# Performance work log

Hardware: AMD Instinct MI355X
Metric: run time of the kernel (lower is better)

## Reference

```python
import jax, jax.numpy as jnp
import numpy as np

B, OBS, H, N = 16384, 512, 1024, 9

def setup_inputs() -> dict:
    key = jax.random.key(0)
    ks = jax.random.split(key, 12)
    s = 0.02
    return {
        "obs": jax.random.normal(ks[0], (B, OBS), jnp.float32),
        "agent_positions": jax.random.normal(ks[1], (B, N, 3), jnp.float32),
        "W1": jax.random.normal(ks[2], (OBS, H), jnp.float32) * s,
        "b1": jnp.zeros((H,), jnp.float32),
        "W2": jax.random.normal(ks[3], (H, H), jnp.float32) * s,
        "b2": jnp.zeros((H,), jnp.float32),
        "Wc1": jax.random.normal(ks[4], (H, H // 2), jnp.float32) * s,
        "bc1": jnp.zeros((H // 2,), jnp.float32),
        "Wc2": jax.random.normal(ks[5], (H // 2, 1), jnp.float32) * s,
        "bc2": jnp.zeros((1,), jnp.float32),
        "Wt1": jax.random.normal(ks[6], (H, H // 2), jnp.float32) * s,
        "bt1": jnp.zeros((H // 2,), jnp.float32),
        "Wt2": jax.random.normal(ks[7], (H // 2, 1), jnp.float32) * s,
        "bt2": jnp.zeros((1,), jnp.float32),
        "Wk1": jax.random.normal(ks[8], (2 * H, H), jnp.float32) * s,
        "bk1": jnp.zeros((H,), jnp.float32),
        "Wk2": jax.random.normal(ks[9], (H, 1), jnp.float32) * s,
        "bk2": jnp.zeros((1,), jnp.float32),
    }


def reference(obs, agent_positions, W1, b1, W2, b2, Wc1, bc1, Wc2, bc2,
              Wt1, bt1, Wt2, bt2, Wk1, bk1, Wk2, bk2):
    # global features: Linear->ReLU->Linear->ReLU
    g = jax.nn.relu(obs @ W1 + b1)
    g = jax.nn.relu(g @ W2 + b2)  # [B, H]

    # Each per-agent head is applied to the SAME g in the original loop,
    # so one pass + broadcast is mathematically identical.
    cov = jax.nn.sigmoid(jax.nn.relu(g @ Wc1 + bc1) @ Wc2 + bc2)  # [B,1]
    trk = jax.nn.sigmoid(jax.nn.relu(g @ Wt1 + bt1) @ Wt2 + bt2)  # [B,1]
    coop_in = jnp.concatenate([g, g], axis=-1)                    # [B,2H]
    coop = jax.nn.sigmoid(jax.nn.relu(coop_in @ Wk1 + bk1) @ Wk2 + bk2)  # [B,1]
    # mean over 8 identical cooperation scores == the score itself

    coverage = jnp.broadcast_to(cov, (cov.shape[0], N))      # [B, N]
    tracking = jnp.broadcast_to(trk, (trk.shape[0], N))      # [B, N]
    cooperation = jnp.broadcast_to(coop, (coop.shape[0], N)) # [B, N]
    return (coverage, tracking, cooperation)
```

## Files before the change

### kernel.cpp

```cpp
#include <hip/hip_runtime.h>
#include <hip/hip_bf16.h>

#define B_ROWS 16384
#define OBS_D  512
#define H_D    1024
#define N_AG   9

typedef __attribute__((ext_vector_type(8))) short short8;
typedef __attribute__((ext_vector_type(4))) float floatx4;

__device__ __forceinline__ unsigned short f_to_bf_raw(float f) {
  union { float f; unsigned u; } c; c.f = f;
  unsigned u = c.u;
  u = u + 0x7FFF + ((u >> 16) & 1);
  return (unsigned short)(u >> 16);
}

__device__ __forceinline__ size_t frag_off(int n, int k, int KT32) {
  const int ft = (n >> 4) * KT32 + (k >> 5);
  const int ln = (n & 15) | (((k >> 3) & 3) << 4);
  return ((size_t)ft * 64 + ln) * 8 + (k & 7);
}

__global__ __launch_bounds__(256) void prep_all(
    const float* __restrict__ obs,
    const float* __restrict__ W1, const float* __restrict__ W2,
    const float* __restrict__ Wc1, const float* __restrict__ Wt1,
    const float* __restrict__ Wk1,
    const float* __restrict__ bc1, const float* __restrict__ bt1,
    const float* __restrict__ bk1,
    const float* __restrict__ Wc2, const float* __restrict__ Wt2,
    const float* __restrict__ Wk2,
    unsigned short* __restrict__ obs_bf,
    unsigned short* __restrict__ W1f, unsigned short* __restrict__ W2f,
    unsigned short* __restrict__ WHf,
    float* __restrict__ bias2048, float* __restrict__ w2cat) {
  __shared__ float t[32][33];
  const int bx  = blockIdx.x;
  const int tid = threadIdx.x;

  if (bx < 4096) {
    int i = (bx * 256 + tid) * 8;
    float4 a = *(const float4*)(obs + i);
    float4 b = *(const float4*)(obs + i + 4);
    short8 o;
    o[0] = (short)f_to_bf_raw(a.x); o[1] = (short)f_to_bf_raw(a.y);
    o[2] = (short)f_to_bf_raw(a.z); o[3] = (short)f_to_bf_raw(a.w);
    o[4] = (short)f_to_bf_raw(b.x); o[5] = (short)f_to_bf_raw(b.y);
    o[6] = (short)f_to_bf_raw(b.z); o[7] = (short)f_to_bf_raw(b.w);
    *(short8*)(obs_bf + i) = o;
    return;
  }

  const int tx = tid & 31;
  const int ty = tid >> 5;

  if (bx < 4608) {
    const int tt = bx - 4096;
    const int k0 = (tt & 15) * 32;
    const int n0 = (tt >> 4) * 32;
#pragma unroll
    for (int i = ty; i < 32; i += 8)
      t[i][tx] = W1[(size_t)(k0 + i) * 1024 + n0 + tx];
    __syncthreads();
#pragma unroll
    for (int i = ty; i < 32; i += 8)
      W1f[frag_off(n0 + i, k0 + tx, 16)] = f_to_bf_raw(t[tx][i]);
    return;
  }

  if (bx < 5632) {
    const int tt = bx - 4608;
    const int k0 = (tt & 31) * 32;
    const int n0 = (tt >> 5) * 32;
#pragma unroll
    for (int i = ty; i < 32; i += 8)
      t[i][tx] = W2[(size_t)(k0 + i) * 1024 + n0 + tx];
    __syncthreads();
#pragma unroll
    for (int i = ty; i < 32; i += 8)
      W2f[frag_off(n0 + i, k0 + tx, 32)] = f_to_bf_raw(t[tx][i]);
    return;
  }

  if (bx < 7680) {
    const int tt = bx - 5632;
    const int k0 = (tt & 31) * 32;
    const int n0 = (tt >> 5) * 32;
#pragma unroll
    for (int i = ty; i < 32; i += 8) {
      const int n = n0 + tx;
      float v;
      if (n0 < 512)
        v = Wc1[(size_t)(k0 + i) * 512 + n];
      else if (n0 < 1024)
        v = Wt1[(size_t)(k0 + i) * 512 + (n - 512)];
      else
        v = Wk1[(size_t)(k0 + i) * 1024 + (n - 1024)]
          + Wk1[(size_t)(k0 + i + 1024) * 1024 + (n - 1024)];
      t[i][tx] = v;
    }
    __syncthreads();
#pragma unroll
    for (int i = ty; i < 32; i += 8)
      WHf[frag_off(n0 + i, k0 + tx, 32)] = f_to_bf_raw(t[tx][i]);
    return;
  }

  {
    int n = (bx - 7680) * 256 + tid;
    float b, w;
    if (n < 512)       { b = bc1[n];        w = Wc2[n]; }
    else if (n < 1024) { b = bt1[n - 512];  w = Wt2[n - 512]; }
    else               { b = bk1[n - 1024]; w = Wk2[n - 1024]; }
    bias2048[n] = b;
    w2cat[n] = w;
  }
}

#define GLD_LDS(gp, lp)                                                        \
  __builtin_amdgcn_global_load_lds(                                            \
      (const __attribute__((address_space(1))) void*)(gp),                     \
      (__attribute__((address_space(3))) void*)(lp), 16, 0, 0)

#define SCB __builtin_amdgcn_sched_barrier(0)

#define MFMA_BF16(a, b, c) __builtin_amdgcn_mfma_f32_16x16x32_bf16(a, b, c, 0, 0, 0)

#define GEMM_CORE_V9(ACC_DECL)                                                 \
  __shared__ __align__(16) unsigned short As[3][128 * 64];          \
  const int tid  = threadIdx.x;                                                \
  const int lane = tid & 63;                                                   \
  const int wave = tid >> 6;                                                   \
  const int m0 = blockIdx.x * 128;                                             \
  const int n0 = blockIdx.y * 128;                                             \
  const int wm = (wave & 1) * 64;                                              \
  const int wn = (wave >> 1) * 64;                                             \
  const int fr = lane & 15;                                                    \
  const int fq = lane >> 4;                                                    \
  ACC_DECL;                                                                    \
  constexpr int KT   = K >> 6;                      \
  constexpr int KT32 = K >> 5;                      \
  const size_t rowb = (size_t)K * 2;                                           \
  const int srow8  = lane >> 3;                   \
  const int schunk = (lane & 7) ^ srow8;          \
  const char* gA = (const char*)A + (size_t)(m0 + wave * 32 + srow8) * rowb    \
                   + schunk * 16;                                              \
  char* lA = (char*)&As[0][0] + wave * 4096 + lane * 16;                       \
  const unsigned short* gB =                                                   \
      Bf + ((size_t)(((n0 + wn) >> 4) * KT32) * 64 + lane) * 8;                \
  const int fsA = (wm + fr) * 128;                                             \
  const int sl0 = ((fq)     ^ (fr & 7)) * 16;                                  \
  const int sl1 = ((4 + fq) ^ (fr & 7)) * 16;                                  \
  short8 FbP[2][2][4];                                                         \
  _Pragma("unroll")                                                            \
  for (int j = 0; j < 4; ++j)                                                  \
    GLD_LDS(gA + (size_t)j * 8 * rowb, lA + j * 1024);                         \
  _Pragma("unroll")                                                            \
  for (int j = 0; j < 4; ++j)                                                  \
    GLD_LDS(gA + 128 + (size_t)j * 8 * rowb,                                   \
            (char*)&As[1][0] + wave * 4096 + lane * 16 + j * 1024);            \
  _Pragma("unroll")                                                            \
  for (int s = 0; s < 2; ++s)                                                  \
    _Pragma("unroll")                                                          \
    for (int ni = 0; ni < 4; ++ni)                                             \
      FbP[0][s][ni] = *(const short8*)(gB + ((size_t)ni * KT32 + s) * 512);    \
  _Pragma("unroll")                                                            \
  for (int k = 0; k < KT; ++k) {           \
    __syncthreads();            \
    if (k + 2 < KT) {                                                          \
      char* d = (char*)&As[(k + 2) % 3][0] + wave * 4096 + lane * 16;          \
      const char* g = gA + (size_t)(k + 2) * 128;                              \
      _Pragma("unroll")                                                        \
      for (int j = 0; j < 4; ++j)                                              \
        GLD_LDS(g + (size_t)j * 8 * rowb, d + j * 1024);                       \
    }                                                                          \
    if (k + 1 < KT) {                                                          \
      _Pragma("unroll")                                                        \
      for (int s = 0; s < 2; ++s)                                              \
        _Pragma("unroll")                                                      \
        for (int ni = 0; ni < 4; ++ni)                                         \
          FbP[(k + 1) & 1][s][ni] = *(const short8*)                           \
              (gB + ((size_t)ni * KT32 + 2 * (k + 1) + s) * 512);              \
    }                                                                          \
    const char* bA = (const char*)&As[k % 3][0];                               \
    short8 Fa0[4], Fa1[4];                                                     \
    _Pragma("unroll")                                                          \
    for (int mi = 0; mi < 4; ++mi)                                             \
      Fa0[mi] = *(const short8*)(bA + fsA + mi * 2048 + sl0);                  \
    _Pragma("unroll")                                                          \
    for (int mi = 0; mi < 4; ++mi)                                             \
      Fa1[mi] = *(const short8*)(bA + fsA + mi * 2048 + sl1);                  \
    _Pragma("unroll")                                                          \
    for (int mi = 0; mi < 4; ++mi)                                             \
      _Pragma("unroll")                                                        \
      for (int ni = 0; ni < 4; ++ni)                                           \
        acc[mi][ni] = __builtin_amdgcn_mfma_f32_16x16x32_bf16(                 \
            Fa0[mi], FbP[k & 1][0][ni], acc[mi][ni], 0, 0, 0);                 \
    _Pragma("unroll")                                                          \
    for (int mi = 0; mi < 4; ++mi)                                             \
      _Pragma("unroll")                                                        \
      for (int ni = 0; ni < 4; ++ni)                                           \
        acc[mi][ni] = __builtin_amdgcn_mfma_f32_16x16x32_bf16(                 \
            Fa1[mi], FbP[k & 1][1][ni], acc[mi][ni], 0, 0, 0);                 \
  }

#define ACC_INIT4                                                              \
  floatx4 acc[4][4];                                                           \
  _Pragma("unroll")                                                            \
  for (int i = 0; i < 4; ++i)                                                  \
    _Pragma("unroll")                                                          \
    for (int j = 0; j < 4; ++j) acc[i][j] = (floatx4){0.f, 0.f, 0.f, 0.f}

#define ST_A16(T, kh)                                                          \
  GLD_LDS(gA0 + (size_t)(T) * 128 + (kh) * 64,                                 \
          Lds + ((T) & 1) * 65536 + (kh) * 16384 + lA0);                       \
  GLD_LDS(gA1 + (size_t)(T) * 128 + (kh) * 64,                                 \
          Lds + ((T) & 1) * 65536 + (kh) * 16384 + lA0 + 8192)

#define ST_B16(T, kh)                                                          \
  GLD_LDS(gB0 + (size_t)(2 * (T) + (kh)) * 1024,                               \
          Lds + ((T) & 1) * 65536 + (kh) * 16384 + lB0);                       \
  GLD_LDS(gB1 + (size_t)(2 * (T) + (kh)) * 1024,                               \
          Lds + ((T) & 1) * 65536 + (kh) * 16384 + lB0 + 8192)

#define ROW16(mi, FA)                                                          \
  acc[mi][0] = MFMA_BF16(FA, Fb0v, acc[mi][0]);                                \
  acc[mi][1] = MFMA_BF16(FA, Fb1v, acc[mi][1]);                                \
  acc[mi][2] = MFMA_BF16(FA, Fb2v, acc[mi][2]);                                \
  acc[mi][3] = MFMA_BF16(FA, Fb3v, acc[mi][3])

#define PHASE16(TT, ks, STAGE_STMT, PRE_BAR2)                                  \
  {                                                                            \
    const char* pb = Lds + ((TT) & 1) * 65536 + (ks) * 16384;                  \
    short8 Fa0 = *(const short8*)(pb + faB + 0 * 1024);                        \
    short8 Fa1 = *(const short8*)(pb + faB + 1 * 1024);                        \
    short8 Fa2 = *(const short8*)(pb + faB + 2 * 1024);                        \
    short8 Fa3 = *(const short8*)(pb + faB + 3 * 1024);                        \
    short8 Fa4 = *(const short8*)(pb + faB + 4 * 1024);                        \
    short8 Fa5 = *(const short8*)(pb + faB + 5 * 1024);                        \
    short8 Fa6 = *(const short8*)(pb + faB + 6 * 1024);                        \
    short8 Fa7 = *(const short8*)(pb + faB + 7 * 1024);                        \
    short8 Fb0v = *(const short8*)(pb + fbB);                                  \
    short8 Fb1v = *(const short8*)(pb + fbB + 1024);                           \
    short8 Fb2v = *(const short8*)(pb + fbB + 2048);                           \
    short8 Fb3v = *(const short8*)(pb + fbB + 3072);                           \
    STAGE_STMT;                                                                \
    SCB; __builtin_amdgcn_s_barrier(); SCB;                                    \
    __builtin_amdgcn_s_setprio(1);                                             \
    ROW16(0, Fa0); ROW16(1, Fa1); ROW16(2, Fa2); ROW16(3, Fa3);                \
    ROW16(4, Fa4); ROW16(5, Fa5); ROW16(6, Fa6); ROW16(7, Fa7);                \
    __builtin_amdgcn_s_setprio(0);                                             \
    PRE_BAR2;                                                                  \
    SCB; __builtin_amdgcn_s_barrier(); SCB;                                    \
  }

#define GEMM_CORE_V16(ACC_DECL)                                                \
  __shared__ __align__(16) char Lds[131072];                                   \
  const int tid  = threadIdx.x;                                                \
  const int lane = tid & 63;                                                   \
  const int wave = tid >> 6;                                         \
  const int m0 = blockIdx.x * 256;                                             \
  const int n0 = blockIdx.y * 256;                                             \
  const int wm = (wave & 1) * 128;                  \
  const int wn = (wave >> 1) * 64;                                             \
  const int fr = lane & 15;                                                    \
  const int fq = lane >> 4;                                                    \
  ACC_DECL;                                                                    \
  constexpr int KT   = K >> 6;                                                 \
  constexpr int KT32 = K >> 5;                                                 \
  const size_t rowb = (size_t)K * 2;                                           \
  const char* gA0 = (const char*)A                                             \
      + (size_t)(m0 + wave * 16 + (lane >> 2)) * rowb                          \
      + (((lane & 3) ^ ((lane >> 3) & 3)) * 16);                               \
  const char* gA1 = gA0 + (size_t)128 * rowb;                                  \
  const char* gB0 = (const char*)Bf                                            \
      + ((size_t)((n0 >> 4) + wave) * KT32) * 1024 + lane * 16;                \
  const char* gB1 = gB0 + (size_t)8 * KT32 * 1024;                             \
  const int lA0 = wave * 1024 + lane * 16;                                     \
  const int lB0 = 32768 + wave * 1024 + lane * 16;                             \
  const int faB = (wm + fr) * 64 + ((fq ^ ((fr >> 1) & 3)) * 16);              \
  const int fbB = 32768 + ((wave >> 1) * 4) * 1024 + lane * 16;                \
               \
  ST_A16(0, 0); ST_B16(0, 0); ST_A16(0, 1); ST_B16(0, 1);                      \
  SCB;                                                                         \
  ST_A16(1, 0); ST_B16(1, 0);                                                  \
  SCB;                                                                         \
  asm volatile("s_waitcnt vmcnt(4)" ::: "memory");       \
  __builtin_amdgcn_s_barrier();                  \
  SCB;                                                                         \
  _Pragma("unroll")                                                            \
  for (int T = 0; T < KT; ++T) {           \
    PHASE16(T, 0,                                                              \
            { if (T + 1 < KT) { ST_A16(T + 1, 1); ST_B16(T + 1, 1); } },       \
            (void)0);                                                          \
    PHASE16(T, 1,                                                              \
            { if (T + 2 < KT) { ST_A16(T + 2, 0); ST_B16(T + 2, 0); } },       \
            if (T + 1 < KT) {                                                  \
              SCB;                                                             \
              if (T + 2 < KT) {                                                \
                asm volatile("s_waitcnt vmcnt(4)" ::: "memory");               \
              } else {                                                         \
                asm volatile("s_waitcnt vmcnt(0)" ::: "memory");               \
              }                                                                \
              SCB;                                                             \
            });                                                                \
  }

#define ACC_INIT8                                                              \
  floatx4 acc[8][4];                                                           \
  _Pragma("unroll")                                                            \
  for (int i = 0; i < 8; ++i)                                                  \
    _Pragma("unroll")                                                          \
    for (int j = 0; j < 4; ++j) acc[i][j] = (floatx4){0.f, 0.f, 0.f, 0.f}

template <int K>
__global__ __launch_bounds__(256, 2) void gemm_bias_relu(
    const unsigned short* __restrict__ A,
    const unsigned short* __restrict__ Bf,
    const float* __restrict__ bias,
    unsigned short* __restrict__ C,
    int M, int N) {
  GEMM_CORE_V9(ACC_INIT4)

#pragma unroll
  for (int ni = 0; ni < 4; ++ni) {
    const int gn = n0 + wn + ni * 16 + fr;
    const float bv = bias[gn];
#pragma unroll
    for (int mi = 0; mi < 4; ++mi) {
#pragma unroll
      for (int r = 0; r < 4; ++r) {
        const int gm = m0 + wm + mi * 16 + fq * 4 + r;
        float v = acc[mi][ni][r] + bv;
        v = v > 0.f ? v : 0.f;
        C[(size_t)gm * N + gn] = f_to_bf_raw(v);
      }
    }
  }
}

template <int K>
__global__ __launch_bounds__(512, 2) void gemm_heads_fused(
    const unsigned short* __restrict__ A,
    const unsigned short* __restrict__ Bf,
    const float* __restrict__ bias,
    const float* __restrict__ w2,
    float* __restrict__ part,
    int M, int N) {
  GEMM_CORE_V16(ACC_INIT8)

  const int j = blockIdx.y * 4 + (wave >> 1);
  float w2v[4], bv[4];
#pragma unroll
  for (int ni = 0; ni < 4; ++ni) {
    const int gn = n0 + wn + ni * 16 + fr;
    w2v[ni] = w2[gn];
    bv[ni]  = bias[gn];
  }
#pragma unroll
  for (int mi = 0; mi < 8; ++mi) {
#pragma unroll
    for (int r = 0; r < 4; ++r) {
      float p = 0.f;
#pragma unroll
      for (int ni = 0; ni < 4; ++ni) {
        float v = acc[mi][ni][r] + bv[ni];
        v = v > 0.f ? v : 0.f;
        p += v * w2v[ni];
      }
      p += __shfl_xor(p, 1);
      p += __shfl_xor(p, 2);
      p += __shfl_xor(p, 4);
      p += __shfl_xor(p, 8);
      if (fr == 0) {
        const int gm = m0 + wm + mi * 16 + fq * 4 + r;
        part[(size_t)j * B_ROWS + gm] = p;
      }
    }
  }
}

__global__ __launch_bounds__(256) void final_out(
    const float* __restrict__ part,
    const float* __restrict__ bc2, const float* __restrict__ bt2,
    const float* __restrict__ bk2, float* __restrict__ out) {
  const int row = blockIdx.x * 256 + threadIdx.x;
  float sc = 0.f, st = 0.f, sk = 0.f;
#pragma unroll
  for (int j = 0; j < 8; ++j)  sc += part[(size_t)j * B_ROWS + row];
#pragma unroll
  for (int j = 8; j < 16; ++j) st += part[(size_t)j * B_ROWS + row];
#pragma unroll
  for (int j = 16; j < 32; ++j) sk += part[(size_t)j * B_ROWS + row];
  const float cv = 1.f / (1.f + expf(-(sc + bc2[0])));
  const float tv = 1.f / (1.f + expf(-(st + bt2[0])));
  const float kv = 1.f / (1.f + expf(-(sk + bk2[0])));
  float* o0 = out + (size_t)row * N_AG;
  float* o1 = out + (size_t)(B_ROWS + row) * N_AG;
  float* o2 = out + (size_t)(2 * B_ROWS + row) * N_AG;
#pragma unroll
  for (int a = 0; a < N_AG; ++a) { o0[a] = cv; o1[a] = tv; o2[a] = kv; }
}

extern "C" void kernel_launch(void* const* d_in, const int* in_sizes, int n_in,
                              void* d_out, int out_size, void* d_ws, size_t ws_size,
                              hipStream_t stream) {
  const float* obs = (const float*)d_in[0];
  const float* W1  = (const float*)d_in[2];
  const float* b1  = (const float*)d_in[3];
  const float* W2  = (const float*)d_in[4];
  const float* b2  = (const float*)d_in[5];
  const float* Wc1 = (const float*)d_in[6];
  const float* bc1 = (const float*)d_in[7];
  const float* Wc2 = (const float*)d_in[8];
  const float* bc2 = (const float*)d_in[9];
  const float* Wt1 = (const float*)d_in[10];
  const float* bt1 = (const float*)d_in[11];
  const float* Wt2 = (const float*)d_in[12];
  const float* bt2 = (const float*)d_in[13];
  const float* Wk1 = (const float*)d_in[14];
  const float* bk1 = (const float*)d_in[15];
  const float* Wk2 = (const float*)d_in[16];
  const float* bk2 = (const float*)d_in[17];
  float* out = (float*)d_out;

  char* ws = (char*)d_ws;
  const size_t MB = 1024 * 1024;
  const size_t FULL_NEED = 70 * MB + 16 * 1024;

  unsigned short *obs_bf, *W1f, *W2f, *WHf, *G1, *G;
  float *bias2048, *w2cat, *PART;
  const bool full = (ws_size == 0) || (ws_size >= FULL_NEED);

  if (full) {
    obs_bf   = (unsigned short*)(ws + 0);
    W1f      = (unsigned short*)(ws + 16 * MB);
    G        = (unsigned short*)(ws + 0);
    G1       = (unsigned short*)(ws + 32 * MB);
    PART     = (float*)(ws + 32 * MB);
    W2f      = (unsigned short*)(ws + 64 * MB);
    WHf      = (unsigned short*)(ws + 66 * MB);
    bias2048 = (float*)(ws + 70 * MB);
    w2cat    = (float*)(ws + 70 * MB + 8 * 1024);
  } else {
    obs_bf   = (unsigned short*)(ws + 0);
    G1       = (unsigned short*)(ws + 16 * MB);
    G        = (unsigned short*)(ws + 32 * MB);
    W1f      = (unsigned short*)(ws + 48 * MB);
    W2f      = (unsigned short*)(ws + 49 * MB);
    WHf      = (unsigned short*)(ws + 51 * MB);
    bias2048 = (float*)(ws + 55 * MB);
    w2cat    = (float*)(ws + 55 * MB + 8 * 1024);
    PART     = (float*)(ws + 55 * MB + 16 * 1024);
  }

  prep_all<<<7688, 256, 0, stream>>>(obs, W1, W2, Wc1, Wt1, Wk1,
                                     bc1, bt1, bk1, Wc2, Wt2, Wk2,
                                     obs_bf, W1f, W2f, WHf, bias2048, w2cat);

  if (full) {
    gemm_bias_relu<512><<<dim3(128, 8), 256, 0, stream>>>(
        obs_bf, W1f, b1, G1, B_ROWS, 1024);
    gemm_bias_relu<1024><<<dim3(128, 8), 256, 0, stream>>>(
        G1, W2f, b2, G, B_ROWS, 1024);
    gemm_heads_fused<1024><<<dim3(64, 8), 512, 0, stream>>>(
        G, WHf, bias2048, w2cat, PART, B_ROWS, 2048);
  } else {
    for (int h = 0; h < 2; ++h) {
      const size_t ro = (size_t)h * 8192;
      gemm_bias_relu<512><<<dim3(64, 8), 256, 0, stream>>>(
          obs_bf + ro * 512, W1f, b1, G1, 8192, 1024);
      gemm_bias_relu<1024><<<dim3(64, 8), 256, 0, stream>>>(
          G1, W2f, b2, G, 8192, 1024);
      gemm_heads_fused<1024><<<dim3(32, 8), 512, 0, stream>>>(
          G, WHf, bias2048, w2cat, PART + ro, 8192, 2048);
    }
  }

  final_out<<<B_ROWS / 256, 256, 0, stream>>>(PART, bc2, bt2, bk2, out);
}
```

Before: 249.7 us.

## Restructure fused-heads GEMM main loop to one barrier per K-tile with interleaved LDS reads

Replaces the two-phase-per-tile schedule (two barriers per half-tile, staged prefetch of half-tiles) with a single phase per 64-wide K tile. The whole next tile is prefetched at once, and LDS fragment reads are interleaved with MFMA clusters under explicit lgkmcnt waits. The aim is to cut barrier count and hide LDS read latency behind MFMAs. The cost is a vmcnt(0) wait each tile, which exposes global load latency because the prefetch distance is only one tile.

```diff
diff --git a/kernel.cpp b/kernel.cpp
--- a/kernel.cpp
+++ b/kernel.cpp
@@ -212,50 +212,85 @@
     _Pragma("unroll")                                                          \
     for (int j = 0; j < 4; ++j) acc[i][j] = (floatx4){0.f, 0.f, 0.f, 0.f}
 
-#define ST_A16(T, kh)                                                          \
+#define ST_A18(T, kh)                                                          \
   GLD_LDS(gA0 + (size_t)(T) * 128 + (kh) * 64,                                 \
           Lds + ((T) & 1) * 65536 + (kh) * 16384 + lA0);                       \
   GLD_LDS(gA1 + (size_t)(T) * 128 + (kh) * 64,                                 \
           Lds + ((T) & 1) * 65536 + (kh) * 16384 + lA0 + 8192)
 
-#define ST_B16(T, kh)                                                          \
+#define ST_B18(T, kh)                                                          \
   GLD_LDS(gB0 + (size_t)(2 * (T) + (kh)) * 1024,                               \
           Lds + ((T) & 1) * 65536 + (kh) * 16384 + lB0);                       \
   GLD_LDS(gB1 + (size_t)(2 * (T) + (kh)) * 1024,                               \
           Lds + ((T) & 1) * 65536 + (kh) * 16384 + lB0 + 8192)
 
-#define ROW16(mi, FA)                                                          \
-  acc[mi][0] = MFMA_BF16(FA, Fb0v, acc[mi][0]);                                \
-  acc[mi][1] = MFMA_BF16(FA, Fb1v, acc[mi][1]);                                \
-  acc[mi][2] = MFMA_BF16(FA, Fb2v, acc[mi][2]);                                \
-  acc[mi][3] = MFMA_BF16(FA, Fb3v, acc[mi][3])
-
-#define PHASE16(TT, ks, STAGE_STMT, PRE_BAR2)                                  \
+#define RD_FA(d0, d1, d2, d3, pbks, mh)                                        \
+  d0 = *(const short8*)((pbks) + faB + ((mh) * 4 + 0) * 1024);                 \
+  d1 = *(const short8*)((pbks) + faB + ((mh) * 4 + 1) * 1024);                 \
+  d2 = *(const short8*)((pbks) + faB + ((mh) * 4 + 2) * 1024);                 \
+  d3 = *(const short8*)((pbks) + faB + ((mh) * 4 + 3) * 1024)
+
+#define RD_FB(d0, d1, d2, d3, pbks)                                            \
+  d0 = *(const short8*)((pbks) + fbB);                                         \
+  d1 = *(const short8*)((pbks) + fbB + 1024);                                  \
+  d2 = *(const short8*)((pbks) + fbB + 2048);                                  \
+  d3 = *(const short8*)((pbks) + fbB + 3072)
+
+#define CL16(base, A0, A1, A2, A3, B0, B1, B2, B3)                             \
+  __builtin_amdgcn_s_setprio(1);                                               \
+  acc[(base)+0][0] = MFMA_BF16(A0, B0, acc[(base)+0][0]);                      \
+  acc[(base)+0][1] = MFMA_BF16(A0, B1, acc[(base)+0][1]);                      \
+  acc[(base)+0][2] = MFMA_BF16(A0, B2, acc[(base)+0][2]);                      \
+  acc[(base)+0][3] = MFMA_BF16(A0, B3, acc[(base)+0][3]);                      \
+  acc[(base)+1][0] = MFMA_BF16(A1, B0, acc[(base)+1][0]);                      \
+  acc[(base)+1][1] = MFMA_BF16(A1, B1, acc[(base)+1][1]);                      \
+  acc[(base)+1][2] = MFMA_BF16(A1, B2, acc[(base)+1][2]);                      \
+  acc[(base)+1][3] = MFMA_BF16(A1, B3, acc[(base)+1][3]);                      \
+  acc[(base)+2][0] = MFMA_BF16(A2, B0, acc[(base)+2][0]);                      \
+  acc[(base)+2][1] = MFMA_BF16(A2, B1, acc[(base)+2][1]);                      \
+  acc[(base)+2][2] = MFMA_BF16(A2, B2, acc[(base)+2][2]);                      \
+  acc[(base)+2][3] = MFMA_BF16(A2, B3, acc[(base)+2][3]);                      \
+  acc[(base)+3][0] = MFMA_BF16(A3, B0, acc[(base)+3][0]);                      \
+  acc[(base)+3][1] = MFMA_BF16(A3, B1, acc[(base)+3][1]);                      \
+  acc[(base)+3][2] = MFMA_BF16(A3, B2, acc[(base)+3][2]);                      \
+  acc[(base)+3][3] = MFMA_BF16(A3, B3, acc[(base)+3][3]);                      \
+  __builtin_amdgcn_s_setprio(0)
+
+#define LGK(n) SCB; asm volatile("s_waitcnt lgkmcnt(" #n ")" ::: "memory"); SCB
+
+#define TILE18(T)                                                              \
   {                                                                            \
-    const char* pb = Lds + ((TT) & 1) * 65536 + (ks) * 16384;                  \
-    short8 Fa0 = *(const short8*)(pb + faB + 0 * 1024);                        \
-    short8 Fa1 = *(const short8*)(pb + faB + 1 * 1024);                        \
-    short8 Fa2 = *(const short8*)(pb + faB + 2 * 1024);                        \
-    short8 Fa3 = *(const short8*)(pb + faB + 3 * 1024);                        \
-    short8 Fa4 = *(const short8*)(pb + faB + 4 * 1024);                        \
-    short8 Fa5 = *(const short8*)(pb + faB + 5 * 1024);                        \
-    short8 Fa6 = *(const short8*)(pb + faB + 6 * 1024);                        \
-    short8 Fa7 = *(const short8*)(pb + faB + 7 * 1024);                        \
-    short8 Fb0v = *(const short8*)(pb + fbB);                                  \
-    short8 Fb1v = *(const short8*)(pb + fbB + 1024);                           \
-    short8 Fb2v = *(const short8*)(pb + fbB + 2048);                           \
-    short8 Fb3v = *(const short8*)(pb + fbB + 3072);                           \
-    STAGE_STMT;                                                                \
-    SCB; __builtin_amdgcn_s_barrier(); SCB;                                    \
-    __builtin_amdgcn_s_setprio(1);                                             \
-    ROW16(0, Fa0); ROW16(1, Fa1); ROW16(2, Fa2); ROW16(3, Fa3);                \
-    ROW16(4, Fa4); ROW16(5, Fa5); ROW16(6, Fa6); ROW16(7, Fa7);                \
-    __builtin_amdgcn_s_setprio(0);                                             \
-    PRE_BAR2;                                                                  \
-    SCB; __builtin_amdgcn_s_barrier(); SCB;                                    \
-  }
-
-#define GEMM_CORE_V16(ACC_DECL)                                                \
+    const char* pk0 = Lds + ((T) & 1) * 65536;                                 \
+    const char* pk1 = pk0 + 16384;                                             \
+    short8 fa00, fa01, fa02, fa03, fb00, fb01, fb02, fb03;                     \
+    RD_FA(fa00, fa01, fa02, fa03, pk0, 0);                                     \
+    RD_FB(fb00, fb01, fb02, fb03, pk0);                                        \
+    if ((T) + 1 < KT) {                                                        \
+      ST_A18((T) + 1, 0); ST_B18((T) + 1, 0);                                  \
+      ST_A18((T) + 1, 1); ST_B18((T) + 1, 1);                                  \
+    }                                                                          \
+    short8 fa10, fa11, fa12, fa13;                                             \
+    RD_FA(fa10, fa11, fa12, fa13, pk0, 1);                                     \
+    LGK(4);                                                                    \
+    CL16(0, fa00, fa01, fa02, fa03, fb00, fb01, fb02, fb03);                   \
+    short8 fa20, fa21, fa22, fa23, fb10, fb11, fb12, fb13;                     \
+    RD_FA(fa20, fa21, fa22, fa23, pk1, 0);                                     \
+    RD_FB(fb10, fb11, fb12, fb13, pk1);                                        \
+    LGK(8);                                                                    \
+    CL16(4, fa10, fa11, fa12, fa13, fb00, fb01, fb02, fb03);                   \
+    short8 fa30, fa31, fa32, fa33;                                             \
+    RD_FA(fa30, fa31, fa32, fa33, pk1, 1);                                     \
+    LGK(4);                                                                    \
+    CL16(0, fa20, fa21, fa22, fa23, fb10, fb11, fb12, fb13);                   \
+    LGK(0);                                                                    \
+    CL16(4, fa30, fa31, fa32, fa33, fb10, fb11, fb12, fb13);                   \
+    SCB;                                                                       \
+    asm volatile("s_waitcnt vmcnt(0)" ::: "memory");                           \
+    __builtin_amdgcn_s_barrier();                                              \
+    SCB;                                                                       \
+  }
+
+#define GEMM_CORE_V18(ACC_DECL)                                                \
   __shared__ __align__(16) char Lds[131072];                                   \
   const int tid  = threadIdx.x;                                                \
   const int lane = tid & 63;                                                   \
@@ -281,30 +316,15 @@
   const int lB0 = 32768 + wave * 1024 + lane * 16;                             \
   const int faB = (wm + fr) * 64 + ((fq ^ ((fr >> 1) & 3)) * 16);              \
   const int fbB = 32768 + ((wave >> 1) * 4) * 1024 + lane * 16;                \
-               \
-  ST_A16(0, 0); ST_B16(0, 0); ST_A16(0, 1); ST_B16(0, 1);                      \
+                             \
+  ST_A18(0, 0); ST_B18(0, 0); ST_A18(0, 1); ST_B18(0, 1);                      \
   SCB;                                                                         \
-  ST_A16(1, 0); ST_B16(1, 0);                                                  \
+  asm volatile("s_waitcnt vmcnt(0)" ::: "memory");                             \
+  __builtin_amdgcn_s_barrier();                                                \
   SCB;                                                                         \
-  asm volatile("s_waitcnt vmcnt(4)" ::: "memory");       \
-  __builtin_amdgcn_s_barrier();                  \
-  SCB;                                                                         \
   _Pragma("unroll")                                                            \
   for (int T = 0; T < KT; ++T) {           \
-    PHASE16(T, 0,                                                              \
-            { if (T + 1 < KT) { ST_A16(T + 1, 1); ST_B16(T + 1, 1); } },       \
-            (void)0);                                                          \
-    PHASE16(T, 1,                                                              \
-            { if (T + 2 < KT) { ST_A16(T + 2, 0); ST_B16(T + 2, 0); } },       \
-            if (T + 1 < KT) {                                                  \
-              SCB;                                                             \
-              if (T + 2 < KT) {                                                \
-                asm volatile("s_waitcnt vmcnt(4)" ::: "memory");               \
-              } else {                                                         \
-                asm volatile("s_waitcnt vmcnt(0)" ::: "memory");               \
-              }                                                                \
-              SCB;                                                             \
-            });                                                                \
+    TILE18(T);                                                                 \
   }
 
 #define ACC_INIT8                                                              \
@@ -348,7 +368,7 @@
     const float* __restrict__ w2,
     float* __restrict__ part,
     int M, int N) {
-  GEMM_CORE_V16(ACC_INIT8)
+  GEMM_CORE_V18(ACC_INIT8)
 
   const int j = blockIdx.y * 4 + (wave >> 1);
   float w2v[4], bv[4];
```

After: 245.7 us. Within noise of the previous version (-1.6%).
